# Kernel optimization log

Measured on AMD Instinct MI355X. Metric: run time of the kernel, lower is better.

Reference implementation:

```python
import jax, jax.numpy as jnp
import numpy as np

N = 50000      # nodes
E = 800000     # edges
F_IN = 128     # input feature dim
HID = 64       # hidden_channels
HEADS = 4      # num_heads
HD = HEADS * HID
NS = 0.2       # leaky_relu negative_slope
EPS = 1e-5     # batchnorm eps


def setup_inputs() -> dict:
    key = jax.random.key(0)
    ks = jax.random.split(key, 20)
    rn = lambda k, shp, sc=0.05: jax.random.normal(k, shp, jnp.float32) * sc
    inp = {}
    inp['x'] = jax.random.normal(ks[0], (N, F_IN), jnp.float32)
    inp['edge_index'] = jax.random.randint(ks[1], (2, E), 0, N, dtype=jnp.int32)
    inp['edge_attr'] = jax.random.uniform(ks[2], (E, 1), dtype=jnp.float32)
    # GATConv layer 0: in=F_IN, out=HID per head, concat=True
    inp['W0'] = rn(ks[3], (F_IN, HD)); inp['as0'] = rn(ks[4], (HEADS, HID)); inp['ad0'] = rn(ks[5], (HEADS, HID)); inp['b0'] = jnp.zeros((HD,), jnp.float32)
    # GATConv layer 1: in=HD, concat=True
    inp['W1'] = rn(ks[6], (HD, HD)); inp['as1'] = rn(ks[7], (HEADS, HID)); inp['ad1'] = rn(ks[8], (HEADS, HID)); inp['b1'] = jnp.zeros((HD,), jnp.float32)
    # GATConv layer 2: in=HD, concat=False (heads averaged)
    inp['W2'] = rn(ks[9], (HD, HD)); inp['as2'] = rn(ks[10], (HEADS, HID)); inp['ad2'] = rn(ks[11], (HEADS, HID)); inp['b2'] = jnp.zeros((HID,), jnp.float32)
    # BatchNorm affine params
    inp['g0'] = jnp.ones((HD,), jnp.float32); inp['be0'] = jnp.zeros((HD,), jnp.float32)
    inp['g1'] = jnp.ones((HD,), jnp.float32); inp['be1'] = jnp.zeros((HD,), jnp.float32)
    inp['g2'] = jnp.ones((HID,), jnp.float32); inp['be2'] = jnp.zeros((HID,), jnp.float32)
    # Edge MLP: (3*HID+1) -> 2*HID -> HID -> 1
    inp['Wm1'] = rn(ks[12], (3 * HID + 1, 2 * HID)); inp['bm1'] = jnp.zeros((2 * HID,), jnp.float32)
    inp['Wm2'] = rn(ks[13], (2 * HID, HID)); inp['bm2'] = jnp.zeros((HID,), jnp.float32)
    inp['Wm3'] = rn(ks[14], (HID, 1)); inp['bm3'] = jnp.zeros((1,), jnp.float32)
    return inp


def _gat(x, src, dst, W, a_s, a_d, b, concat):
    """PyG GATConv: gather -> linear -> attention -> segment softmax -> scatter-add.
    Adds self-loops (PyG default)."""
    n = x.shape[0]
    H, D = a_s.shape
    h = (x @ W).reshape(n, H, D)                       # [N, H, D]
    loop = jnp.arange(n, dtype=src.dtype)
    s = jnp.concatenate([src, loop])                   # [E+N]
    d = jnp.concatenate([dst, loop])
    alpha_src = jnp.einsum('nhd,hd->nh', h, a_s)       # [N, H]
    alpha_dst = jnp.einsum('nhd,hd->nh', h, a_d)
    e = jax.nn.leaky_relu(alpha_src[s] + alpha_dst[d], NS)   # [E+N, H]
    # numerically stable segment softmax over incoming edges per dst node
    m = jax.ops.segment_max(e, d, num_segments=n)
    ex = jnp.exp(e - m[d])
    den = jax.ops.segment_sum(ex, d, num_segments=n)
    att = ex / den[d]                                  # [E+N, H]
    out = jax.ops.segment_sum(h[s] * att[:, :, None], d, num_segments=n)  # [N, H, D]
    if concat:
        return out.reshape(n, H * D) + b
    return out.mean(axis=1) + b


def _bn(x, g, b):
    # BatchNorm1d, training-mode statistics (biased variance), deterministic
    mu = x.mean(axis=0)
    var = x.var(axis=0)
    return (x - mu) * jax.lax.rsqrt(var + EPS) * g + b


def reference(x, edge_index, edge_attr,
              W0, as0, ad0, b0, g0, be0,
              W1, as1, ad1, b1, g1, be1,
              W2, as2, ad2, b2, g2, be2,
              Wm1, bm1, Wm2, bm2, Wm3, bm3):
    src, dst = edge_index[0], edge_index[1]
    h = _gat(x, src, dst, W0, as0, ad0, b0, True)
    h = jax.nn.leaky_relu(_bn(h, g0, be0), NS)
    h = _gat(h, src, dst, W1, as1, ad1, b1, True)
    h = jax.nn.leaky_relu(_bn(h, g1, be1), NS)
    h = _gat(h, src, dst, W2, as2, ad2, b2, False)
    h = _bn(h, g2, be2)                                # [N, HID]
    hs, hd = h[src], h[dst]                            # gathers: [E, HID]
    ef = jnp.concatenate([hs, hd, jnp.abs(hs - hd), edge_attr], axis=1)  # [E, 3*HID+1]
    ef = jax.nn.leaky_relu(ef @ Wm1 + bm1, NS)
    ef = jax.nn.leaky_relu(ef @ Wm2 + bm2, NS)
    return (ef @ Wm3 + bm3).squeeze(-1)                # [E] edge logits
```

## Files before the change

kernel.cpp:

```cpp
#include <hip/hip_runtime.h>
#include <math.h>

#define Nn 50000
#define Npad 50048
#define Ee 800000
#define FIN 128
#define HIDd 64
#define NH 4
#define HD 256
#define NEG 0.2f
#define BEPS 1e-5f

typedef __attribute__((ext_vector_type(8))) short short8;
typedef __attribute__((ext_vector_type(4))) float f32x4;
typedef unsigned int uint;
typedef unsigned short ushort;

static __device__ __forceinline__ float lrelu(float x) { return x > 0.f ? x : NEG * x; }
static __device__ __forceinline__ float bf2f(ushort x) {
  return __uint_as_float(((uint)x) << 16);
}
static __device__ __forceinline__ ushort f2bf(float f) {
  uint u = __float_as_uint(f);
  return (ushort)((u + 0x7FFF + ((u >> 16) & 1)) >> 16);
}

__global__ void fill_kernel(float* __restrict__ p, float v, int n) {
  int i = blockIdx.x * 256 + threadIdx.x;
  if (i < n) p[i] = v;
}

__global__ void filli_kernel(int* __restrict__ p, int v, int n) {
  int i = blockIdx.x * 256 + threadIdx.x;
  if (i < n) p[i] = v;
}

__global__ void hist_kernel(const int* __restrict__ dst, int* __restrict__ deg) {
  int i = blockIdx.x * 256 + threadIdx.x;
  if (i < Ee) atomicAdd(&deg[dst[i]], 1);
}

__global__ __launch_bounds__(1024) void scan_kernel(const int* __restrict__ deg,
                                                    int* __restrict__ rowstart) {
  __shared__ int ts[1024];
  const int tid = threadIdx.x;
  const int CH = (Nn + 1023) / 1024;
  const int base = tid * CH;
  int s = 0;
  for (int j = 0; j < CH; j++) {
    int idx = base + j;
    if (idx < Nn) s += deg[idx];
  }
  ts[tid] = s;
  __syncthreads();
  for (int off = 1; off < 1024; off <<= 1) {
    int v = (tid >= off) ? ts[tid - off] : 0;
    __syncthreads();
    ts[tid] += v;
    __syncthreads();
  }
  int run = (tid == 0) ? 0 : ts[tid - 1];
  for (int j = 0; j < CH; j++) {
    int idx = base + j;
    if (idx < Nn) {
      rowstart[idx] = run;
      run += deg[idx];
      if (idx == Nn - 1) rowstart[Nn] = run;
    }
  }
}

__global__ void cursor_init_kernel(const int* __restrict__ rowstart, int* __restrict__ cursor) {
  int i = blockIdx.x * 256 + threadIdx.x;
  if (i < Nn) cursor[i] = rowstart[i];
}

__global__ void elist_fill_kernel(const int* __restrict__ src, const int* __restrict__ dst,
                                  int* __restrict__ cursor, int* __restrict__ elist) {
  int i = blockIdx.x * 256 + threadIdx.x;
  if (i >= Ee + Nn) return;
  int s, d;
  if (i < Ee) { s = src[i]; d = dst[i]; } else { s = d = i - Ee; }
  int pos = atomicAdd(&cursor[d], 1);
  elist[pos] = s;
}

__global__ void cvt_bf16_kernel(const float* __restrict__ in, ushort* __restrict__ out, int n) {
  int i = blockIdx.x * 256 + threadIdx.x;
  if (i < n) out[i] = f2bf(in[i]);
}

__global__ void wfrag_kernel(const float* __restrict__ W, ushort* __restrict__ Wf, int K) {
  int idx = blockIdx.x * 256 + threadIdx.x;
  int total = (K >> 5) * 16 * 64 * 8;
  if (idx >= total) return;
  int j = idx & 7, lane = (idx >> 3) & 63, t = (idx >> 9) & 15, kc = idx >> 13;
  int n = t * 16 + (lane & 15);
  int k = kc * 32 + ((lane >> 4) << 3) + j;
  Wf[idx] = f2bf(W[k * 256 + n]);
}

__global__ __launch_bounds__(256) void gemm_mfma_kernel(
    const ushort* __restrict__ A, const ushort* __restrict__ Bf, ushort* __restrict__ Chm, int K,
    const float* __restrict__ a_s, const float* __restrict__ a_d,
    float* __restrict__ asrc, float* __restrict__ adst) {
  const int tid = threadIdx.x;
  const int w = tid >> 6, lane = tid & 63;
  const int q = lane >> 4, nn = lane & 15;
  const int m0 = blockIdx.x * 128 + w * 32;
  const int cb = blockIdx.y;
  f32x4 acc[2][8];
#pragma unroll
  for (int tm = 0; tm < 2; tm++)
#pragma unroll
    for (int t = 0; t < 8; t++) acc[tm][t] = (f32x4){0.f, 0.f, 0.f, 0.f};
  const int nkc = K >> 5;
  for (int kc = 0; kc < nkc; kc++) {
    short8 a0 = *(const short8*)(A + (size_t)(m0 + nn) * K + kc * 32 + q * 8);
    short8 a1 = *(const short8*)(A + (size_t)(m0 + 16 + nn) * K + kc * 32 + q * 8);
#pragma unroll
    for (int t = 0; t < 8; t++) {
      short8 b = *(const short8*)(Bf + ((size_t)((kc * 16 + cb * 8 + t) * 64 + lane)) * 8);
      acc[0][t] = __builtin_amdgcn_mfma_f32_16x16x32_bf16(a0, b, acc[0][t], 0, 0, 0);
      acc[1][t] = __builtin_amdgcn_mfma_f32_16x16x32_bf16(a1, b, acc[1][t], 0, 0, 0);
    }
  }
  float asv[8], adv[8];
#pragma unroll
  for (int t = 0; t < 8; t++) {
    int head = 2 * cb + (t >> 2);
    int dim = (t & 3) * 16 + nn;
    asv[t] = a_s[head * 64 + dim];
    adv[t] = a_d[head * 64 + dim];
  }
#pragma unroll
  for (int tm = 0; tm < 2; tm++) {
    float ps[2][4] = {{0.f, 0.f, 0.f, 0.f}, {0.f, 0.f, 0.f, 0.f}};
    float pd[2][4] = {{0.f, 0.f, 0.f, 0.f}, {0.f, 0.f, 0.f, 0.f}};
#pragma unroll
    for (int t = 0; t < 8; t++) {
      int hp = t >> 2;
      int head = 2 * cb + hp;
      int dim = (t & 3) * 16 + nn;
#pragma unroll
      for (int r = 0; r < 4; r++) {
        float v = acc[tm][t][r];
        int row = m0 + tm * 16 + q * 4 + r;
        Chm[((size_t)head * Npad + row) * 64 + dim] = f2bf(v);
        ps[hp][r] = fmaf(v, asv[t], ps[hp][r]);
        pd[hp][r] = fmaf(v, adv[t], pd[hp][r]);
      }
    }
#pragma unroll
    for (int hp = 0; hp < 2; hp++)
#pragma unroll
      for (int r = 0; r < 4; r++) {
        float s = ps[hp][r], d2 = pd[hp][r];
        s += __shfl_xor(s, 1); s += __shfl_xor(s, 2);
        s += __shfl_xor(s, 4); s += __shfl_xor(s, 8);
        d2 += __shfl_xor(d2, 1); d2 += __shfl_xor(d2, 2);
        d2 += __shfl_xor(d2, 4); d2 += __shfl_xor(d2, 8);
        if (nn == 0) {
          int row = m0 + tm * 16 + q * 4 + r;
          asrc[row * 4 + 2 * cb + hp] = s;
          adst[row * 4 + 2 * cb + hp] = d2;
        }
      }
  }
}

__global__ __launch_bounds__(64) void gat_gather_kernel(
    const int* __restrict__ elist, const int* __restrict__ rowstart,
    const ushort* __restrict__ h, const float* __restrict__ asrc,
    const float* __restrict__ adst, const float* __restrict__ bias,
    ushort* __restrict__ aggb, float* __restrict__ aggf, int concat) {
  const int n = blockIdx.x;
  const int hh = blockIdx.y;
  const int lane = threadIdx.x;
  const int start = rowstart[n], end = rowstart[n + 1];
  const float adstv = adst[n * 4 + hh];
  const ushort* hbase = h + ((size_t)hh * Npad) * 64 + lane;
  float acc = 0.f, den = 0.f;
  int j = start;
  for (; j + 3 < end; j += 4) {
    int s0 = elist[j], s1 = elist[j + 1], s2 = elist[j + 2], s3 = elist[j + 3];
    float e0 = asrc[s0 * 4 + hh] + adstv;
    float e1 = asrc[s1 * 4 + hh] + adstv;
    float e2 = asrc[s2 * 4 + hh] + adstv;
    float e3 = asrc[s3 * 4 + hh] + adstv;
    ushort v0 = hbase[(size_t)s0 * 64];
    ushort v1 = hbase[(size_t)s1 * 64];
    ushort v2 = hbase[(size_t)s2 * 64];
    ushort v3 = hbase[(size_t)s3 * 64];
    float w0 = __expf(lrelu(e0)), w1 = __expf(lrelu(e1));
    float w2 = __expf(lrelu(e2)), w3 = __expf(lrelu(e3));
    den += (w0 + w1) + (w2 + w3);
    acc = fmaf(w0, bf2f(v0), acc);
    acc = fmaf(w1, bf2f(v1), acc);
    acc = fmaf(w2, bf2f(v2), acc);
    acc = fmaf(w3, bf2f(v3), acc);
  }
  for (; j < end; j++) {
    int s0 = elist[j];
    float e0 = asrc[s0 * 4 + hh] + adstv;
    ushort v0 = hbase[(size_t)s0 * 64];
    float w0 = __expf(lrelu(e0));
    den += w0;
    acc = fmaf(w0, bf2f(v0), acc);
  }
  float o = acc / den;
  const int col = hh * 64 + lane;
  if (concat) {
    aggb[(size_t)n * HD + col] = f2bf(o + bias[col]);
  } else {
    aggf[(size_t)n * HD + col] = o;
  }
}

__global__ void mean_heads_kernel(const float* __restrict__ agg, const float* __restrict__ b,
                                  float* __restrict__ h2) {
  int i = blockIdx.x * 256 + threadIdx.x;
  if (i >= Nn * HIDd) return;
  int n = i >> 6, dd = i & 63;
  const float* r = agg + (size_t)n * HD + dd;
  h2[i] = 0.25f * (r[0] + r[64] + r[128] + r[192]) + b[dd];
}

__global__ void bn_stats_bf16_kernel(const ushort* __restrict__ x, float* __restrict__ stats,
                                     int nrows, int C) {
  int r0 = blockIdx.x * 512;
  int tpc = 256 / C;
  int c = threadIdx.x % C;
  int ro = threadIdx.x / C;
  int rend = min(r0 + 512, nrows);
  float s = 0.f, s2 = 0.f;
  for (int r = r0 + ro; r < rend; r += tpc) {
    float v = bf2f(x[(size_t)r * C + c]);
    s += v; s2 += v * v;
  }
  atomicAdd(&stats[c], s);
  atomicAdd(&stats[C + c], s2);
}

__global__ void bn_stats_kernel(const float* __restrict__ x, float* __restrict__ stats,
                                int nrows, int C) {
  int r0 = blockIdx.x * 512;
  int tpc = 256 / C;
  int c = threadIdx.x % C;
  int ro = threadIdx.x / C;
  int rend = min(r0 + 512, nrows);
  float s = 0.f, s2 = 0.f;
  for (int r = r0 + ro; r < rend; r += tpc) {
    float v = x[(size_t)r * C + c];
    s += v; s2 += v * v;
  }
  atomicAdd(&stats[c], s);
  atomicAdd(&stats[C + c], s2);
}

__global__ void bn_apply_inplace_kernel(ushort* __restrict__ x, const float* __restrict__ stats,
                                        const float* __restrict__ g, const float* __restrict__ be,
                                        int C) {
  int i = blockIdx.x * 256 + threadIdx.x;
  if (i >= Nn * C) return;
  int c = i % C;
  float mu = stats[c] * (1.f / Nn);
  float var = stats[C + c] * (1.f / Nn) - mu * mu;
  float y = (bf2f(x[i]) - mu) * rsqrtf(var + BEPS) * g[c] + be[c];
  x[i] = f2bf(lrelu(y));
}

__global__ void bn_apply_bf16_kernel(const float* __restrict__ x, const float* __restrict__ stats,
                                     const float* __restrict__ g, const float* __restrict__ be,
                                     ushort* __restrict__ outb, int C) {
  int i = blockIdx.x * 256 + threadIdx.x;
  if (i >= Nn * C) return;
  int c = i % C;
  float mu = stats[c] * (1.f / Nn);
  float var = stats[C + c] * (1.f / Nn) - mu * mu;
  float y = (x[i] - mu) * rsqrtf(var + BEPS) * g[c] + be[c];
  outb[i] = f2bf(y);
}

__global__ void w1frag_kernel(const float* __restrict__ Wm1, ushort* __restrict__ W1f) {
  int idx = blockIdx.x * 256 + threadIdx.x;
  if (idx >= 7 * 8 * 64 * 8) return;
  int j = idx & 7, lane = (idx >> 3) & 63, tile = (idx >> 9) & 7, chunk = idx >> 12;
  int n = tile * 16 + (lane & 15);
  int k = chunk * 32 + (lane >> 4) * 8 + j;
  W1f[idx] = (k < 193) ? f2bf(Wm1[k * 128 + n]) : (ushort)0;
}

__global__ void w2frag_kernel(const float* __restrict__ Wm2, ushort* __restrict__ W2f) {
  int idx = blockIdx.x * 256 + threadIdx.x;
  if (idx >= 4 * 4 * 64 * 8) return;
  int j = idx & 7, lane = (idx >> 3) & 63, tile = (idx >> 9) & 3, chunk = idx >> 11;
  int n = tile * 16 + (lane & 15);
  int k = chunk * 32 + (lane >> 4) * 8 + j;
  W2f[idx] = f2bf(Wm2[k * 64 + n]);
}

static __device__ __forceinline__ short8 absdiff8(short8 a, short8 b) {
  short8 r;
#pragma unroll
  for (int j = 0; j < 8; j++) r[j] = (short)f2bf(fabsf(bf2f((ushort)a[j]) - bf2f((ushort)b[j])));
  return r;
}

#define MLP1_STEP(c, e0x, e1x)                                                         \
  {                                                                                    \
    short8 _a0 = (e0x);                                                                \
    short8 _a1 = (e1x);                                                                \
    const uint4* bp = (const uint4*)W1f + (c) * 512 + lane;                            \
    _Pragma("unroll") for (int t = 0; t < 8; t++) {                                    \
      uint4 braw = bp[t * 64];                                                         \
      short8 b = *(short8*)&braw;                                                      \
      acc0[t] = __builtin_amdgcn_mfma_f32_16x16x32_bf16(_a0, b, acc0[t], 0, 0, 0);     \
      acc1[t] = __builtin_amdgcn_mfma_f32_16x16x32_bf16(_a1, b, acc1[t], 0, 0, 0);     \
    }                                                                                  \
  }

__global__ __launch_bounds__(256) void edge_mlp_mfma_kernel(
    const ushort* __restrict__ hb, const int* __restrict__ src, const int* __restrict__ dst,
    const float* __restrict__ eattr, const ushort* __restrict__ W1f,
    const ushort* __restrict__ W2f, const float* __restrict__ bm1,
    const float* __restrict__ bm2, const float* __restrict__ Wm3,
    const float* __restrict__ bm3, float* __restrict__ out) {
  __shared__ ushort t1s[4][16 * 136];
  const int tid = threadIdx.x;
  const int w = tid >> 6, lane = tid & 63;
  const int q = lane >> 4, nn = lane & 15;

  float bm1v[8];
#pragma unroll
  for (int t = 0; t < 8; t++) bm1v[t] = bm1[t * 16 + nn];
  float bm2v[4], w3v[4];
#pragma unroll
  for (int t = 0; t < 4; t++) { bm2v[t] = bm2[t * 16 + nn]; w3v[t] = Wm3[t * 16 + nn]; }
  const float bm3v = bm3[0];

  const int base = blockIdx.x * 128 + w * 32;
  const int e0 = base + nn, e1 = base + 16 + nn;
  const int s0 = src[e0], d0 = dst[e0];
  const int s1 = src[e1], d1 = dst[e1];
  const float at0 = eattr[e0], at1 = eattr[e1];

  short8 hs0a = *(const short8*)(hb + s0 * 64 + q * 8);
  short8 hs0b = *(const short8*)(hb + s0 * 64 + 32 + q * 8);
  short8 hd0a = *(const short8*)(hb + d0 * 64 + q * 8);
  short8 hd0b = *(const short8*)(hb + d0 * 64 + 32 + q * 8);
  short8 hs1a = *(const short8*)(hb + s1 * 64 + q * 8);
  short8 hs1b = *(const short8*)(hb + s1 * 64 + 32 + q * 8);
  short8 hd1a = *(const short8*)(hb + d1 * 64 + q * 8);
  short8 hd1b = *(const short8*)(hb + d1 * 64 + 32 + q * 8);

  f32x4 acc0[8], acc1[8];
#pragma unroll
  for (int t = 0; t < 8; t++) {
    acc0[t] = (f32x4){0.f, 0.f, 0.f, 0.f};
    acc1[t] = (f32x4){0.f, 0.f, 0.f, 0.f};
  }

  short8 a6_0 = 0, a6_1 = 0;
  if (q == 0) { a6_0[0] = (short)f2bf(at0); a6_1[0] = (short)f2bf(at1); }

  MLP1_STEP(0, hs0a, hs1a)
  MLP1_STEP(1, hs0b, hs1b)
  MLP1_STEP(2, hd0a, hd1a)
  MLP1_STEP(3, hd0b, hd1b)
  MLP1_STEP(4, absdiff8(hs0a, hd0a), absdiff8(hs1a, hd1a))
  MLP1_STEP(5, absdiff8(hs0b, hd0b), absdiff8(hs1b, hd1b))
  MLP1_STEP(6, a6_0, a6_1)

  ushort* myt1 = t1s[w];
  auto do_group = [&](f32x4* acc, int g) {
#pragma unroll
    for (int t = 0; t < 8; t++)
#pragma unroll
      for (int r = 0; r < 4; r++)
        myt1[(q * 4 + r) * 136 + t * 16 + nn] = f2bf(lrelu(acc[t][r] + bm1v[t]));
    f32x4 acc2[4];
#pragma unroll
    for (int t = 0; t < 4; t++) acc2[t] = (f32x4){0.f, 0.f, 0.f, 0.f};
#pragma unroll
    for (int c2 = 0; c2 < 4; c2++) {
      short8 a = *(short8*)&myt1[nn * 136 + c2 * 32 + q * 8];
#pragma unroll
      for (int t = 0; t < 4; t++) {
        short8 b = *(const short8*)(W2f + ((size_t)(c2 * 4 + t) * 64 + lane) * 8);
        acc2[t] = __builtin_amdgcn_mfma_f32_16x16x32_bf16(a, b, acc2[t], 0, 0, 0);
      }
    }
#pragma unroll
    for (int r = 0; r < 4; r++) {
      float sum = 0.f;
#pragma unroll
      for (int t = 0; t < 4; t++) sum += lrelu(acc2[t][r] + bm2v[t]) * w3v[t];
      sum += __shfl_xor(sum, 1);
      sum += __shfl_xor(sum, 2);
      sum += __shfl_xor(sum, 4);
      sum += __shfl_xor(sum, 8);
      if (nn == 0) out[base + g * 16 + q * 4 + r] = sum + bm3v;
    }
  };
  do_group(acc0, 0);
  do_group(acc1, 1);
}

extern "C" void kernel_launch(void* const* d_in, const int* in_sizes, int n_in,
                              void* d_out, int out_size, void* d_ws, size_t ws_size,
                              hipStream_t stream) {
  const float* x    = (const float*)d_in[0];
  const int*   ei   = (const int*)d_in[1];
  const float* eatt = (const float*)d_in[2];
  const float* W0 = (const float*)d_in[3];
  const float* as0 = (const float*)d_in[4];
  const float* ad0 = (const float*)d_in[5];
  const float* b0 = (const float*)d_in[6];
  const float* W1 = (const float*)d_in[7];
  const float* as1 = (const float*)d_in[8];
  const float* ad1 = (const float*)d_in[9];
  const float* b1 = (const float*)d_in[10];
  const float* W2 = (const float*)d_in[11];
  const float* as2 = (const float*)d_in[12];
  const float* ad2 = (const float*)d_in[13];
  const float* b2 = (const float*)d_in[14];
  const float* g0 = (const float*)d_in[15];
  const float* be0 = (const float*)d_in[16];
  const float* g1 = (const float*)d_in[17];
  const float* be1 = (const float*)d_in[18];
  const float* g2 = (const float*)d_in[19];
  const float* be2 = (const float*)d_in[20];
  const float* Wm1 = (const float*)d_in[21];
  const float* bm1 = (const float*)d_in[22];
  const float* Wm2 = (const float*)d_in[23];
  const float* bm2 = (const float*)d_in[24];
  const float* Wm3 = (const float*)d_in[25];
  const float* bm3 = (const float*)d_in[26];
  const int* src = ei;
  const int* dst = ei + Ee;
  float* out = (float*)d_out;

  char* w = (char*)d_ws;
  float*  agg  = (float*)w;
  ushort* xb   = (ushort*)w;
  ushort* hB   = (ushort*)(w + (size_t)Npad * 256 * 4);
  float*  h2   = (float*)hB;
  ushort* aggb = (ushort*)(w + (size_t)Npad * 256 * 6);
  ushort* hb2  = aggb;
  float*  asrc = (float*)(w + (size_t)Npad * 256 * 8);
  float*  adst = asrc + (size_t)Npad * 4;
  float*  stats = adst + (size_t)Npad * 4;
  int* deg      = (int*)(stats + 512);
  int* rowstart = deg + Nn;
  int* cursor   = rowstart + Nn + 16;
  int* elist    = cursor + Nn;
  ushort* W0f  = (ushort*)(elist + Ee + Nn);
  ushort* W1gf = W0f + 32768;
  ushort* W2gf = W1gf + 65536;
  ushort* eW1f = W2gf + 65536;
  ushort* eW2f = eW1f + 28672;

  filli_kernel<<<(Nn + 255) / 256, 256, 0, stream>>>(deg, 1, Nn);
  hist_kernel<<<(Ee + 255) / 256, 256, 0, stream>>>(dst, deg);
  scan_kernel<<<1, 1024, 0, stream>>>(deg, rowstart);
  cursor_init_kernel<<<(Nn + 255) / 256, 256, 0, stream>>>(rowstart, cursor);
  elist_fill_kernel<<<(Ee + Nn + 255) / 256, 256, 0, stream>>>(src, dst, cursor, elist);

  wfrag_kernel<<<(32768 + 255) / 256, 256, 0, stream>>>(W0, W0f, FIN);
  wfrag_kernel<<<(65536 + 255) / 256, 256, 0, stream>>>(W1, W1gf, HD);
  wfrag_kernel<<<(65536 + 255) / 256, 256, 0, stream>>>(W2, W2gf, HD);
  w1frag_kernel<<<(7 * 8 * 64 * 8 + 255) / 256, 256, 0, stream>>>(Wm1, eW1f);
  w2frag_kernel<<<(4 * 4 * 64 * 8 + 255) / 256, 256, 0, stream>>>(Wm2, eW2f);

  auto gat = [&](const ushort* Ab, const ushort* Wf, int K, const float* a_s,
                 const float* a_d, const float* bias, bool concat) {
    gemm_mfma_kernel<<<dim3(Npad / 128, 2), 256, 0, stream>>>(Ab, Wf, hB, K, a_s, a_d,
                                                              asrc, adst);
    gat_gather_kernel<<<dim3(Nn, NH), 64, 0, stream>>>(elist, rowstart, hB, asrc, adst, bias,
                                                       aggb, agg, concat ? 1 : 0);
  };

  cvt_bf16_kernel<<<(Nn * FIN + 255) / 256, 256, 0, stream>>>(x, xb, Nn * FIN);
  gat(xb, W0f, FIN, as0, ad0, b0, true);
  fill_kernel<<<2, 256, 0, stream>>>(stats, 0.f, 512);
  bn_stats_bf16_kernel<<<(Nn + 511) / 512, 256, 0, stream>>>(aggb, stats, Nn, HD);
  bn_apply_inplace_kernel<<<(Nn * HD + 255) / 256, 256, 0, stream>>>(aggb, stats, g0, be0, HD);
  gat(aggb, W1gf, HD, as1, ad1, b1, true);
  fill_kernel<<<2, 256, 0, stream>>>(stats, 0.f, 512);
  bn_stats_bf16_kernel<<<(Nn + 511) / 512, 256, 0, stream>>>(aggb, stats, Nn, HD);
  bn_apply_inplace_kernel<<<(Nn * HD + 255) / 256, 256, 0, stream>>>(aggb, stats, g1, be1, HD);
  gat(aggb, W2gf, HD, as2, ad2, b2, false);
  mean_heads_kernel<<<(Nn * HIDd + 255) / 256, 256, 0, stream>>>(agg, b2, h2);
  fill_kernel<<<1, 256, 0, stream>>>(stats, 0.f, 128);
  bn_stats_kernel<<<(Nn + 511) / 512, 256, 0, stream>>>(h2, stats, Nn, HIDd);
  bn_apply_bf16_kernel<<<(Nn * HIDd + 255) / 256, 256, 0, stream>>>(h2, stats, g2, be2, hb2,
                                                                    HIDd);
  edge_mlp_mfma_kernel<<<Ee / 128, 256, 0, stream>>>(hb2, src, dst, eatt, eW1f, eW2f, bm1, bm2,
                                                     Wm3, bm3, out);
}
```

Before: 1.298 ms.

## Store GAT features row-major and gather all heads per node in one wavefront

The GEMM epilogue now writes projected features in node-major [N,256] order instead of head-major planes. The gather kernel then assigns one 64-lane wavefront per destination node, with each lane covering 4 columns through 8-byte loads, and packs 4 nodes into a 256-thread block. Neighbour indices and rowstart are read once per node instead of once per head, and each source row becomes one contiguous 512-byte read. The cursor copy is also folded into the scan kernel, removing one launch. The GEMM stores are now strided per row, which may write less efficiently than before.

```diff
diff --git a/kernel.cpp b/kernel.cpp
--- a/kernel.cpp
+++ b/kernel.cpp
@@ -41,7 +41,8 @@
 }
 
 __global__ __launch_bounds__(1024) void scan_kernel(const int* __restrict__ deg,
-                                                    int* __restrict__ rowstart) {
+                                                    int* __restrict__ rowstart,
+                                                    int* __restrict__ cursor) {
   __shared__ int ts[1024];
   const int tid = threadIdx.x;
   const int CH = (Nn + 1023) / 1024;
@@ -64,15 +65,11 @@
     int idx = base + j;
     if (idx < Nn) {
       rowstart[idx] = run;
+      cursor[idx] = run;
       run += deg[idx];
       if (idx == Nn - 1) rowstart[Nn] = run;
     }
   }
-}
-
-__global__ void cursor_init_kernel(const int* __restrict__ rowstart, int* __restrict__ cursor) {
-  int i = blockIdx.x * 256 + threadIdx.x;
-  if (i < Nn) cursor[i] = rowstart[i];
 }
 
 __global__ void elist_fill_kernel(const int* __restrict__ src, const int* __restrict__ dst,
@@ -101,7 +98,7 @@
 }
 
 __global__ __launch_bounds__(256) void gemm_mfma_kernel(
-    const ushort* __restrict__ A, const ushort* __restrict__ Bf, ushort* __restrict__ Chm, int K,
+    const ushort* __restrict__ A, const ushort* __restrict__ Bf, ushort* __restrict__ C, int K,
     const float* __restrict__ a_s, const float* __restrict__ a_d,
     float* __restrict__ asrc, float* __restrict__ adst) {
   const int tid = threadIdx.x;
@@ -140,13 +137,11 @@
 #pragma unroll
     for (int t = 0; t < 8; t++) {
       int hp = t >> 2;
-      int head = 2 * cb + hp;
-      int dim = (t & 3) * 16 + nn;
 #pragma unroll
       for (int r = 0; r < 4; r++) {
         float v = acc[tm][t][r];
         int row = m0 + tm * 16 + q * 4 + r;
-        Chm[((size_t)head * Npad + row) * 64 + dim] = f2bf(v);
+        C[(size_t)row * 256 + cb * 128 + t * 16 + nn] = f2bf(v);
         ps[hp][r] = fmaf(v, asv[t], ps[hp][r]);
         pd[hp][r] = fmaf(v, adv[t], pd[hp][r]);
       }
@@ -169,18 +164,19 @@
   }
 }
 
-__global__ __launch_bounds__(64) void gat_gather_kernel(
+__global__ __launch_bounds__(256) void gat_gather_kernel(
     const int* __restrict__ elist, const int* __restrict__ rowstart,
     const ushort* __restrict__ h, const float* __restrict__ asrc,
     const float* __restrict__ adst, const float* __restrict__ bias,
     ushort* __restrict__ aggb, float* __restrict__ aggf, int concat) {
-  const int n = blockIdx.x;
-  const int hh = blockIdx.y;
-  const int lane = threadIdx.x;
+  const int n = blockIdx.x * 4 + (threadIdx.x >> 6);
+  const int lane = threadIdx.x & 63;
+  const int hh = lane >> 4;
   const int start = rowstart[n], end = rowstart[n + 1];
   const float adstv = adst[n * 4 + hh];
-  const ushort* hbase = h + ((size_t)hh * Npad) * 64 + lane;
-  float acc = 0.f, den = 0.f;
+  const ushort* hcol = h + lane * 4;
+  float4 acc = make_float4(0.f, 0.f, 0.f, 0.f);
+  float den = 0.f;
   int j = start;
   for (; j + 3 < end; j += 4) {
     int s0 = elist[j], s1 = elist[j + 1], s2 = elist[j + 2], s3 = elist[j + 3];
@@ -188,32 +184,41 @@
     float e1 = asrc[s1 * 4 + hh] + adstv;
     float e2 = asrc[s2 * 4 + hh] + adstv;
     float e3 = asrc[s3 * 4 + hh] + adstv;
-    ushort v0 = hbase[(size_t)s0 * 64];
-    ushort v1 = hbase[(size_t)s1 * 64];
-    ushort v2 = hbase[(size_t)s2 * 64];
-    ushort v3 = hbase[(size_t)s3 * 64];
+    ushort4 v0 = *(const ushort4*)(hcol + (size_t)s0 * HD);
+    ushort4 v1 = *(const ushort4*)(hcol + (size_t)s1 * HD);
+    ushort4 v2 = *(const ushort4*)(hcol + (size_t)s2 * HD);
+    ushort4 v3 = *(const ushort4*)(hcol + (size_t)s3 * HD);
     float w0 = __expf(lrelu(e0)), w1 = __expf(lrelu(e1));
     float w2 = __expf(lrelu(e2)), w3 = __expf(lrelu(e3));
     den += (w0 + w1) + (w2 + w3);
-    acc = fmaf(w0, bf2f(v0), acc);
-    acc = fmaf(w1, bf2f(v1), acc);
-    acc = fmaf(w2, bf2f(v2), acc);
-    acc = fmaf(w3, bf2f(v3), acc);
+    acc.x = fmaf(w0, bf2f(v0.x), acc.x); acc.y = fmaf(w0, bf2f(v0.y), acc.y);
+    acc.z = fmaf(w0, bf2f(v0.z), acc.z); acc.w = fmaf(w0, bf2f(v0.w), acc.w);
+    acc.x = fmaf(w1, bf2f(v1.x), acc.x); acc.y = fmaf(w1, bf2f(v1.y), acc.y);
+    acc.z = fmaf(w1, bf2f(v1.z), acc.z); acc.w = fmaf(w1, bf2f(v1.w), acc.w);
+    acc.x = fmaf(w2, bf2f(v2.x), acc.x); acc.y = fmaf(w2, bf2f(v2.y), acc.y);
+    acc.z = fmaf(w2, bf2f(v2.z), acc.z); acc.w = fmaf(w2, bf2f(v2.w), acc.w);
+    acc.x = fmaf(w3, bf2f(v3.x), acc.x); acc.y = fmaf(w3, bf2f(v3.y), acc.y);
+    acc.z = fmaf(w3, bf2f(v3.z), acc.z); acc.w = fmaf(w3, bf2f(v3.w), acc.w);
   }
   for (; j < end; j++) {
     int s0 = elist[j];
     float e0 = asrc[s0 * 4 + hh] + adstv;
-    ushort v0 = hbase[(size_t)s0 * 64];
+    ushort4 v0 = *(const ushort4*)(hcol + (size_t)s0 * HD);
     float w0 = __expf(lrelu(e0));
     den += w0;
-    acc = fmaf(w0, bf2f(v0), acc);
-  }
-  float o = acc / den;
-  const int col = hh * 64 + lane;
+    acc.x = fmaf(w0, bf2f(v0.x), acc.x); acc.y = fmaf(w0, bf2f(v0.y), acc.y);
+    acc.z = fmaf(w0, bf2f(v0.z), acc.z); acc.w = fmaf(w0, bf2f(v0.w), acc.w);
+  }
+  float inv = 1.f / den;
+  float o0 = acc.x * inv, o1 = acc.y * inv, o2 = acc.z * inv, o3 = acc.w * inv;
   if (concat) {
-    aggb[(size_t)n * HD + col] = f2bf(o + bias[col]);
+    float4 bv = *(const float4*)(bias + lane * 4);
+    ushort4 ov;
+    ov.x = f2bf(o0 + bv.x); ov.y = f2bf(o1 + bv.y);
+    ov.z = f2bf(o2 + bv.z); ov.w = f2bf(o3 + bv.w);
+    *(ushort4*)(aggb + (size_t)n * HD + lane * 4) = ov;
   } else {
-    aggf[(size_t)n * HD + col] = o;
+    *(float4*)(aggf + (size_t)n * HD + lane * 4) = make_float4(o0, o1, o2, o3);
   }
 }
 
@@ -463,8 +468,7 @@
 
   filli_kernel<<<(Nn + 255) / 256, 256, 0, stream>>>(deg, 1, Nn);
   hist_kernel<<<(Ee + 255) / 256, 256, 0, stream>>>(dst, deg);
-  scan_kernel<<<1, 1024, 0, stream>>>(deg, rowstart);
-  cursor_init_kernel<<<(Nn + 255) / 256, 256, 0, stream>>>(rowstart, cursor);
+  scan_kernel<<<1, 1024, 0, stream>>>(deg, rowstart, cursor);
   elist_fill_kernel<<<(Ee + Nn + 255) / 256, 256, 0, stream>>>(src, dst, cursor, elist);
 
   wfrag_kernel<<<(32768 + 255) / 256, 256, 0, stream>>>(W0, W0f, FIN);
@@ -477,8 +481,8 @@
                  const float* a_d, const float* bias, bool concat) {
     gemm_mfma_kernel<<<dim3(Npad / 128, 2), 256, 0, stream>>>(Ab, Wf, hB, K, a_s, a_d,
                                                               asrc, adst);
-    gat_gather_kernel<<<dim3(Nn, NH), 64, 0, stream>>>(elist, rowstart, hB, asrc, adst, bias,
-                                                       aggb, agg, concat ? 1 : 0);
+    gat_gather_kernel<<<Nn / 4, 256, 0, stream>>>(elist, rowstart, hB, asrc, adst, bias,
+                                                  aggb, agg, concat ? 1 : 0);
   };
 
   cvt_bf16_kernel<<<(Nn * FIN + 255) / 256, 256, 0, stream>>>(x, xb, Nn * FIN);
```

After: 1.144 ms. 1.13x faster.
